# Kernel optimization log

Hardware: AMD Instinct MI355X
Metric: run time of the kernel (lower is better)

Reference implementation:

```python
import math
import jax, jax.numpy as jnp
import numpy as np

B, T, H = 4, 2048, 1024
E, K, F = 8, 2, 2048
CAP_FACTOR = 1.25


def setup_inputs() -> dict:
    key = jax.random.key(0)
    k1, k2, k3, k4 = jax.random.split(key, 4)
    x = jax.random.normal(k1, (B, T, H), dtype=jnp.float32)
    Wg = jax.random.normal(k2, (H, E), dtype=jnp.float32) * 0.02
    W_in = jax.random.normal(k3, (E, H, 2 * F), dtype=jnp.float32) * (1.0 / math.sqrt(H))
    W_out = jax.random.normal(k4, (E, F, H), dtype=jnp.float32) * (1.0 / math.sqrt(F))
    return {"x": x, "Wg": Wg, "W_in": W_in, "W_out": W_out}


def _moe_forward(x, Wg, W_in, W_out):
    b, t, h = x.shape
    xf = x.reshape(-1, h)                      # [S, H] flattened tokens
    S = xf.shape[0]
    C = int(math.ceil(K * S / E * CAP_FACTOR))  # per-expert capacity (drop_tokens=True)

    # --- gating (noiseless top-k, eval/RSample-off path) ---
    logits = xf @ Wg                           # [S, E]
    probs = jax.nn.softmax(logits, axis=-1)
    top_vals, top_idx = jax.lax.top_k(probs, K)  # [S, K]

    # --- capacity-ordered locations, slot-major priority (slot0 before slot1) ---
    flat_idx = top_idx.T.reshape(-1)           # [K*S], slot-major
    onehot = jax.nn.one_hot(flat_idx, E, dtype=jnp.int32)
    cum = jnp.cumsum(onehot, axis=0) - 1       # position within each expert
    loc = jnp.take_along_axis(cum, flat_idx[:, None], axis=1)[:, 0]
    loc = loc.reshape(K, S).T                  # [S, K]
    keep = loc < C                             # token-drop mask

    # --- gate weights normalized over kept slots (DeepSpeed top-k normalization) ---
    gates = top_vals * keep.astype(top_vals.dtype)       # [S, K]
    denom = jnp.maximum(gates.sum(-1, keepdims=True), 1e-9)
    gates = gates / denom

    # --- dispatch: scatter tokens into [E, C, H] buffers (pad slot C for drops) ---
    loc_c = jnp.where(keep, loc, C)
    e_flat = top_idx.reshape(-1)               # [S*K]
    l_flat = loc_c.reshape(-1)
    xk = jnp.broadcast_to(xf[:, None, :], (S, K, h)).reshape(-1, h)
    xk = jnp.where(keep.reshape(-1, 1), xk, 0.0)
    buf = jnp.zeros((E, C + 1, h), x.dtype).at[e_flat, l_flat].set(xk)
    inp = buf[:, :C]                           # [E, C, H]

    # --- GLU experts as grouped GEMMs ---
    hid = jnp.einsum('ech,ehf->ecf', inp, W_in)          # [E, C, 2F]
    a, g = jnp.split(hid, 2, axis=-1)
    hid = jax.nn.gelu(a, approximate=False) * g          # torch gelu = exact erf
    out_e = jnp.einsum('ecf,efh->ech', hid, W_out)       # [E, C, H]

    # --- combine: gather per-slot expert outputs, weight by gates, sum over k ---
    out_pad = jnp.concatenate([out_e, jnp.zeros((E, 1, h), out_e.dtype)], axis=1)
    gathered = out_pad[e_flat, l_flat].reshape(S, K, h)
    y = (gathered * gates[..., None]).sum(axis=1)        # [S, H]
    return y.reshape(b, t, h)


def reference(x, Wg, W_in, W_out):
    return _moe_forward(x, Wg, W_in, W_out)
```

## Files before the change

### kernel.cpp

```cpp
#include <hip/hip_runtime.h>
#include <hip/hip_bf16.h>
#include <math.h>

#define S_TOK 8192
#define HDIM  1024
#define FDIM  2048
#define CAP   2560

typedef unsigned short u16;
typedef short  s16x8 __attribute__((ext_vector_type(8)));
typedef float  f32x4 __attribute__((ext_vector_type(4)));

__device__ __forceinline__ u16 f2b(float f){
  unsigned u = __builtin_bit_cast(unsigned, f);
  u = (u + 0x7FFFu + ((u >> 16) & 1u)) >> 16;
  return (u16)u;
}
__device__ __forceinline__ float b2f(u16 h){
  unsigned u = ((unsigned)h) << 16;
  return __builtin_bit_cast(float, u);
}
__device__ __forceinline__ void gl_lds16(const u16* g, u16* l){
  auto gp = (const __attribute__((address_space(1))) unsigned int*)g;
  auto lp = (__attribute__((address_space(3))) unsigned int*)l;
  __builtin_amdgcn_global_load_lds(gp, lp, 16, 0, 0);
}

__device__ __forceinline__ int glu_reorder(int c){
  int h = (c >= 2048) ? 1 : 0;
  int cc = c - (h << 11);
  return ((cc >> 5) << 6) + (h << 5) + (cc & 31);
}

template<int REORDER>
__global__ __launch_bounds__(256) void k_transpose(const float* __restrict__ in,
                                                   u16* __restrict__ out, int R, int Cc){
  __shared__ float tile[32][33];
  int e = blockIdx.z;
  const float* ip = in + (size_t)e * R * Cc;
  u16* op = out + (size_t)e * R * Cc;
  int c0 = blockIdx.x * 32, r0 = blockIdx.y * 32;
  int tx = threadIdx.x, ty = threadIdx.y;
  #pragma unroll
  for (int j = 0; j < 32; j += 8)
    tile[ty + j][tx] = ip[(size_t)(r0 + ty + j) * Cc + c0 + tx];
  __syncthreads();
  #pragma unroll
  for (int j = 0; j < 32; j += 8){
    int c = c0 + ty + j;
    int rp = REORDER ? glu_reorder(c) : c;
    op[(size_t)rp * R + r0 + tx] = f2b(tile[tx][ty + j]);
  }
}

__global__ __launch_bounds__(256) void k_gating(const float* __restrict__ x,
                                                const float* __restrict__ Wg,
                                                int* __restrict__ eidx, float* __restrict__ vals){
  __shared__ float wgT[8][1024];
  int t = threadIdx.x;
  for (int i = t; i < 8192; i += 256) wgT[i & 7][i >> 3] = Wg[i];
  __syncthreads();
  int wid = t >> 6, l = t & 63;
  int s = blockIdx.x * 4 + wid;
  const float* xr = x + (size_t)s * HDIM;
  double acc[8] = {0,0,0,0,0,0,0,0};
  for (int j = 0; j < 16; j++){
    int h = l + 64 * j;
    float xv = xr[h];
    #pragma unroll
    for (int e = 0; e < 8; e++) acc[e] += (double)xv * (double)wgT[e][h];
  }
  #pragma unroll
  for (int off = 32; off; off >>= 1)
    #pragma unroll
    for (int e = 0; e < 8; e++) acc[e] += __shfl_down(acc[e], off);
  if (l == 0){
    double mx = acc[0];
    #pragma unroll
    for (int e = 1; e < 8; e++) mx = acc[e] > mx ? acc[e] : mx;
    double ex[8], sum = 0.0;
    #pragma unroll
    for (int e = 0; e < 8; e++){ ex[e] = exp(acc[e] - mx); sum += ex[e]; }
    double inv = 1.0 / sum;
    double p0 = -1.0; int e0 = 0;
    #pragma unroll
    for (int e = 0; e < 8; e++){ double p = ex[e] * inv; if (p > p0){ p0 = p; e0 = e; } }
    double p1 = -1.0; int e1 = 0;
    #pragma unroll
    for (int e = 0; e < 8; e++){ double p = ex[e] * inv; if (e != e0 && p > p1){ p1 = p; e1 = e; } }
    eidx[s] = e0;          vals[s] = (float)p0;
    eidx[S_TOK + s] = e1;  vals[S_TOK + s] = (float)p1;
  }
}

__global__ __launch_bounds__(1024) void k_scan(const int* __restrict__ eidx,
                                               const float* __restrict__ vals,
                                               int* __restrict__ slot, float* __restrict__ gates,
                                               int* __restrict__ cnt){
  __shared__ int sc[1024][8];
  __shared__ unsigned char keepb[2 * S_TOK];
  int t = threadIdx.x;
  int le[16];
  int c[8] = {0,0,0,0,0,0,0,0};
  #pragma unroll
  for (int j = 0; j < 16; j++){ int e = eidx[t * 16 + j]; le[j] = e; c[e]++; }
  #pragma unroll
  for (int e = 0; e < 8; e++) sc[t][e] = c[e];
  __syncthreads();
  for (int st = 1; st < 1024; st <<= 1){
    int tmp[8] = {0,0,0,0,0,0,0,0};
    bool act = (t >= st);
    if (act){
      #pragma unroll
      for (int e = 0; e < 8; e++) tmp[e] = sc[t - st][e];
    }
    __syncthreads();
    if (act){
      #pragma unroll
      for (int e = 0; e < 8; e++) sc[t][e] += tmp[e];
    }
    __syncthreads();
  }
  int run[8];
  #pragma unroll
  for (int e = 0; e < 8; e++) run[e] = t ? sc[t - 1][e] : 0;
  #pragma unroll
  for (int j = 0; j < 16; j++){
    int i = t * 16 + j; int e = le[j]; int loc = run[e]++;
    int kp = (loc < CAP);
    keepb[i] = (unsigned char)kp;
    slot[i] = kp ? (e * CAP + loc) : -1;
  }
  if (t < 8) cnt[t] = min(sc[1023][t], CAP);
  __syncthreads();
  #pragma unroll
  for (int r = 0; r < 8; r++){
    int s = t + 1024 * r;
    float g0 = keepb[s]         ? vals[s]         : 0.f;
    float g1 = keepb[S_TOK + s] ? vals[S_TOK + s] : 0.f;
    float inv = 1.f / fmaxf(g0 + g1, 1e-9f);
    gates[s] = g0 * inv;
    gates[S_TOK + s] = g1 * inv;
  }
}

__global__ __launch_bounds__(256) void k_scatter(const float* __restrict__ x,
                                                 const int* __restrict__ slot,
                                                 u16* __restrict__ A){
  int i = blockIdx.x;
  int sl = slot[i];
  if (sl < 0) return;
  int s = i & (S_TOK - 1);
  int t = threadIdx.x;
  float4 v = ((const float4*)(x + (size_t)s * HDIM))[t];
  ushort4 o; o.x = f2b(v.x); o.y = f2b(v.y); o.z = f2b(v.z); o.w = f2b(v.w);
  ((ushort4*)(A + (size_t)sl * HDIM))[t] = o;
}


#define STAGE_A(h, tt, par) { \
    const u16* gp_ = Ap + (size_t)((h)*128 + c0*8) * LDK + (size_t)(tt) * 64 + srow_off; \
    u16* lp_ = lds + (par)*16384 + (h)*8192 + c0*512; \
    gl_lds16(gp_, lp_); gl_lds16(gp_ + (size_t)8*LDK, lp_ + 512); }

#define STAGE_B(h, tt, par) { \
    const u16* gp_ = Bp + (size_t)((h)*128 + c0*8) * LDK + (size_t)(tt) * 64 + srow_off; \
    u16* lp_ = lds + 32768 + (par)*16384 + (h)*8192 + c0*512; \
    gl_lds16(gp_, lp_); gl_lds16(gp_ + (size_t)8*LDK, lp_ + 512); }

#define PH(P, KSW, NH, STAGE_CODE, POST_CODE) { \
    __builtin_amdgcn_sched_barrier(0); \
    if ((NH) == 0) { \
      _Pragma("unroll") \
      for (int m_ = 0; m_ < 8; ++m_) \
        af[m_] = *(const s16x8*)&lds[(P)*16384 + aoff + m_*1024 + (KSW)]; \
    } \
    bf[0] = *(const s16x8*)&lds[32768 + (P)*16384 + boff + (2*(NH))*1024 + (KSW)]; \
    bf[1] = *(const s16x8*)&lds[32768 + (P)*16384 + boff + (2*(NH)+1)*1024 + (KSW)]; \
    STAGE_CODE \
    __builtin_amdgcn_sched_barrier(0); __builtin_amdgcn_s_barrier(); \
    asm volatile("s_waitcnt lgkmcnt(0)" ::: "memory"); \
    __builtin_amdgcn_sched_barrier(0); \
    __builtin_amdgcn_s_setprio(1); \
    _Pragma("unroll") \
    for (int m_ = 0; m_ < 8; ++m_){ \
      acc[m_][2*(NH)]   = __builtin_amdgcn_mfma_f32_16x16x32_bf16(af[m_], bf[0], acc[m_][2*(NH)],   0, 0, 0); \
      acc[m_][2*(NH)+1] = __builtin_amdgcn_mfma_f32_16x16x32_bf16(af[m_], bf[1], acc[m_][2*(NH)+1], 0, 0, 0); \
    } \
    __builtin_amdgcn_s_setprio(0); \
    POST_CODE \
    __builtin_amdgcn_sched_barrier(0); __builtin_amdgcn_s_barrier(); }

template<int NK, int LDK, int NB, int IS_GLU>
__global__ __launch_bounds__(512, 2) void k_gemm8(const u16* __restrict__ Aall,
                                                  const u16* __restrict__ Ball,
                                                  u16* __restrict__ Out,
                                                  const int* __restrict__ cnt){
  int e = blockIdx.z, mt = blockIdx.x, nt = blockIdx.y;
  if (mt * 256 >= cnt[e]) return;
  __shared__ __align__(1024) u16 lds[65536];
  const u16* Ap = Aall + (size_t)e * CAP * LDK + (size_t)mt * 256 * LDK;
  const u16* Bp = Ball + (size_t)e * NB * LDK + (size_t)nt * 256 * LDK;

  const int t = threadIdx.x, wid = t >> 6, l = t & 63;
  const int wm = wid >> 2, wn = wid & 3;
  const int lrow = l & 15, lkhi = l >> 4;
  const int c0 = wid * 2;
  const size_t srow_off = (size_t)(l >> 3) * LDK + (size_t)(((l & 7) * 8) ^ ((l >> 3) * 8));
  const int aoff = wm * 8192 + lrow * 64;
  const int boff = (wn >> 1) * 8192 + ((wn & 1) * 64 + lrow) * 64;
  const int sx   = (l & 7) * 8;
  const int ksw0 = (lkhi * 8) ^ sx;
  const int ksw1 = (32 + lkhi * 8) ^ sx;

  f32x4 acc[8][4] = {};
  s16x8 af[8], bf[2];

  STAGE_A(0, 0, 0) STAGE_A(1, 0, 0) STAGE_B(0, 0, 0) STAGE_B(1, 0, 0)
  STAGE_A(0, 1, 1) STAGE_A(1, 1, 1)
  asm volatile("s_waitcnt vmcnt(4)" ::: "memory");
  __builtin_amdgcn_sched_barrier(0); __builtin_amdgcn_s_barrier();

  #pragma unroll 1
  for (int t2 = 0; t2 < NK / 2; ++t2){
    const int te = 2 * t2;
    const bool nl = (t2 < NK / 2 - 1);
    PH(0, ksw0, 0, { STAGE_B(0, te + 1, 1) }, {})
    PH(0, ksw0, 1, { STAGE_B(1, te + 1, 1) }, {})
    PH(0, ksw1, 0, {}, {})
    PH(0, ksw1, 1,
       { if (nl){ STAGE_A(0, te + 2, 0) STAGE_A(1, te + 2, 0) } },
       { if (nl){ asm volatile("s_waitcnt vmcnt(4)" ::: "memory"); }
         else   { asm volatile("s_waitcnt vmcnt(0)" ::: "memory"); } })
    PH(1, ksw0, 0, { if (nl){ STAGE_B(0, te + 2, 0) } }, {})
    PH(1, ksw0, 1, { if (nl){ STAGE_B(1, te + 2, 0) } }, {})
    PH(1, ksw1, 0, {}, {})
    PH(1, ksw1, 1,
       { if (nl){ STAGE_A(0, te + 3, 1) STAGE_A(1, te + 3, 1) } },
       { if (nl){ asm volatile("s_waitcnt vmcnt(4)" ::: "memory"); } })
  }

  const int rowb = mt * 256 + wm * 128 + lkhi * 4;
  if (IS_GLU){
    u16* hp = Out + (size_t)e * CAP * FDIM;
    const int colb = (nt * 4 + wn) * 32 + lrow;
    #pragma unroll
    for (int m = 0; m < 8; ++m)
      #pragma unroll
      for (int np = 0; np < 2; ++np)
        #pragma unroll
        for (int r = 0; r < 4; ++r){
          size_t row = (size_t)(rowb + m * 16 + r);
          float a = acc[m][np][r], g = acc[m][np + 2][r];
          float h = 0.5f * a * (1.f + erff(a * 0.70710678118f)) * g;
          hp[row * FDIM + colb + np * 16] = f2b(h);
        }
  } else {
    u16* op = Out + (size_t)e * CAP * HDIM;
    const int colb = nt * 256 + wn * 64 + lrow;
    #pragma unroll
    for (int m = 0; m < 8; ++m)
      #pragma unroll
      for (int n = 0; n < 4; ++n)
        #pragma unroll
        for (int r = 0; r < 4; ++r){
          size_t row = (size_t)(rowb + m * 16 + r);
          op[row * HDIM + colb + n * 16] = f2b(acc[m][n][r]);
        }
  }
}

__global__ __launch_bounds__(256) void k_gather(const u16* __restrict__ oute,
                                                const int* __restrict__ slot,
                                                const float* __restrict__ gates,
                                                float* __restrict__ y){
  int s = blockIdx.x, t = threadIdx.x;
  int s0 = slot[s], s1 = slot[S_TOK + s];
  float g0 = gates[s], g1 = gates[S_TOK + s];
  float4 r; r.x = r.y = r.z = r.w = 0.f;
  if (s0 >= 0){
    ushort4 v = ((const ushort4*)(oute + (size_t)s0 * HDIM))[t];
    r.x += g0 * b2f(v.x); r.y += g0 * b2f(v.y); r.z += g0 * b2f(v.z); r.w += g0 * b2f(v.w);
  }
  if (s1 >= 0){
    ushort4 v = ((const ushort4*)(oute + (size_t)s1 * HDIM))[t];
    r.x += g1 * b2f(v.x); r.y += g1 * b2f(v.y); r.z += g1 * b2f(v.z); r.w += g1 * b2f(v.w);
  }
  ((float4*)(y + (size_t)s * HDIM))[t] = r;
}

extern "C" void kernel_launch(void* const* d_in, const int* in_sizes, int n_in,
                              void* d_out, int out_size, void* d_ws, size_t ws_size,
                              hipStream_t stream){
  (void)in_sizes; (void)n_in; (void)out_size; (void)ws_size;
  const float* x     = (const float*)d_in[0];
  const float* Wg    = (const float*)d_in[1];
  const float* W_in  = (const float*)d_in[2];
  const float* W_out = (const float*)d_in[3];
  float* y = (float*)d_out;

  char* ws = (char*)d_ws;
  u16* WiT   = (u16*)(ws);
  u16* WoT   = (u16*)(ws + 67108864);
  u16* Ainp  = (u16*)(ws + 100663296);
  u16* hid   = (u16*)(ws + 142606336);
  int*   eidx  = (int*)  (ws + 226492416);
  float* vals  = (float*)(ws + 226492416 + 65536);
  int*   slot  = (int*)  (ws + 226492416 + 131072);
  float* gates = (float*)(ws + 226492416 + 196608);
  int*   cnt   = (int*)  (ws + 226492416 + 262144);

  k_transpose<1><<<dim3(128, 32, 8), dim3(32, 8), 0, stream>>>(W_in,  WiT, 1024, 4096);
  k_transpose<0><<<dim3(32, 64, 8),  dim3(32, 8), 0, stream>>>(W_out, WoT, 2048, 1024);
  k_gating   <<<dim3(2048), dim3(256),  0, stream>>>(x, Wg, eidx, vals);
  k_scan     <<<dim3(1),    dim3(1024), 0, stream>>>(eidx, vals, slot, gates, cnt);
  k_scatter  <<<dim3(2 * S_TOK), dim3(256), 0, stream>>>(x, slot, Ainp);
  k_gemm8<16, 1024, 4096, 1><<<dim3(10, 16, 8), dim3(512), 0, stream>>>(Ainp, WiT, hid, cnt);
  k_gemm8<32, 2048, 1024, 0><<<dim3(10, 4, 8),  dim3(512), 0, stream>>>(hid, WoT, Ainp, cnt);
  k_gather   <<<dim3(S_TOK), dim3(256), 0, stream>>>(Ainp, slot, gates, y);
}
```

Measured before the change: 644.4 us.

## Fuse combine into down-proj GEMM with atomics, tanh GELU, XCD-aware block remap

Removes the separate gather kernel by having the second GEMM scatter gate-weighted results into y with float atomicAdd, using a reverse slot-to-token map built in the scan kernel and a memset of y. Replaces the exact erf GELU with a tanh approximation. Remaps workgroup IDs so that consecutive tiles are spread across the 8 XCDs for better L2 locality. The atomics add contention and make the result order nondeterministic, and the tanh GELU changes numerics relative to the exact-erf reference.

```diff
diff --git a/kernel.cpp b/kernel.cpp
--- a/kernel.cpp
+++ b/kernel.cpp
@@ -24,6 +24,13 @@
   auto gp = (const __attribute__((address_space(1))) unsigned int*)g;
   auto lp = (__attribute__((address_space(3))) unsigned int*)l;
   __builtin_amdgcn_global_load_lds(gp, lp, 16, 0, 0);
+}
+__device__ __forceinline__ float gelu_t(float a){
+  float z = 0.7978845608f * a * (1.f + 0.044715f * a * a);
+  float e = __expf(-2.f * fabsf(z));
+  float th = (1.f - e) / (1.f + e);
+  th = (z < 0.f) ? -th : th;
+  return 0.5f * a * (1.f + th);
 }
 
 __device__ __forceinline__ int glu_reorder(int c){
@@ -96,7 +103,7 @@
 __global__ __launch_bounds__(1024) void k_scan(const int* __restrict__ eidx,
                                                const float* __restrict__ vals,
                                                int* __restrict__ slot, float* __restrict__ gates,
-                                               int* __restrict__ cnt){
+                                               int* __restrict__ cnt, int* __restrict__ rev){
   __shared__ int sc[1024][8];
   __shared__ unsigned char keepb[2 * S_TOK];
   int t = threadIdx.x;
@@ -129,7 +136,9 @@
     int i = t * 16 + j; int e = le[j]; int loc = run[e]++;
     int kp = (loc < CAP);
     keepb[i] = (unsigned char)kp;
-    slot[i] = kp ? (e * CAP + loc) : -1;
+    int sl = kp ? (e * CAP + loc) : -1;
+    slot[i] = sl;
+    if (kp) rev[sl] = i;
   }
   if (t < 8) cnt[t] = min(sc[1023][t], CAP);
   __syncthreads();
@@ -191,12 +200,23 @@
     POST_CODE \
     __builtin_amdgcn_sched_barrier(0); __builtin_amdgcn_s_barrier(); }
 
-template<int NK, int LDK, int NB, int IS_GLU>
+template<int NK, int LDK, int NB, int IS_GLU, int FUSE>
 __global__ __launch_bounds__(512, 2) void k_gemm8(const u16* __restrict__ Aall,
                                                   const u16* __restrict__ Ball,
                                                   u16* __restrict__ Out,
-                                                  const int* __restrict__ cnt){
-  int e = blockIdx.z, mt = blockIdx.x, nt = blockIdx.y;
+                                                  float* __restrict__ yout,
+                                                  const int* __restrict__ cnt,
+                                                  const int* __restrict__ rev,
+                                                  const float* __restrict__ gates){
+  const int gx = gridDim.x, gy = gridDim.y;
+  const int o = blockIdx.x + gx * (blockIdx.y + gy * blockIdx.z);
+  const int nwg = gx * gy * (int)gridDim.z;
+  const int q = nwg >> 3;
+  const int w = (o & 7) * q + (o >> 3);
+  const int mt = w % gx;
+  const int t1 = w / gx;
+  const int nt = t1 % gy;
+  const int e  = t1 / gy;
   if (mt * 256 >= cnt[e]) return;
   __shared__ __align__(1024) u16 lds[65536];
   const u16* Ap = Aall + (size_t)e * CAP * LDK + (size_t)mt * 256 * LDK;
@@ -252,9 +272,26 @@
         for (int r = 0; r < 4; ++r){
           size_t row = (size_t)(rowb + m * 16 + r);
           float a = acc[m][np][r], g = acc[m][np + 2][r];
-          float h = 0.5f * a * (1.f + erff(a * 0.70710678118f)) * g;
-          hp[row * FDIM + colb + np * 16] = f2b(h);
+          hp[row * FDIM + colb + np * 16] = f2b(gelu_t(a) * g);
         }
+  } else if (FUSE){
+    const int cE = cnt[e];
+    const int colb = nt * 256 + wn * 64 + lrow;
+    #pragma unroll
+    for (int m = 0; m < 8; ++m)
+      #pragma unroll
+      for (int r = 0; r < 4; ++r){
+        int row = rowb + m * 16 + r;
+        if (row < cE){
+          int i = rev[e * CAP + row];
+          float g = gates[i];
+          int s = i & (S_TOK - 1);
+          float* yp = yout + (size_t)s * HDIM + colb;
+          #pragma unroll
+          for (int n = 0; n < 4; ++n)
+            atomicAdd(yp + n * 16, g * acc[m][n][r]);
+        }
+      }
   } else {
     u16* op = Out + (size_t)e * CAP * HDIM;
     const int colb = nt * 256 + wn * 64 + lrow;
@@ -270,29 +307,10 @@
   }
 }
 
-__global__ __launch_bounds__(256) void k_gather(const u16* __restrict__ oute,
-                                                const int* __restrict__ slot,
-                                                const float* __restrict__ gates,
-                                                float* __restrict__ y){
-  int s = blockIdx.x, t = threadIdx.x;
-  int s0 = slot[s], s1 = slot[S_TOK + s];
-  float g0 = gates[s], g1 = gates[S_TOK + s];
-  float4 r; r.x = r.y = r.z = r.w = 0.f;
-  if (s0 >= 0){
-    ushort4 v = ((const ushort4*)(oute + (size_t)s0 * HDIM))[t];
-    r.x += g0 * b2f(v.x); r.y += g0 * b2f(v.y); r.z += g0 * b2f(v.z); r.w += g0 * b2f(v.w);
-  }
-  if (s1 >= 0){
-    ushort4 v = ((const ushort4*)(oute + (size_t)s1 * HDIM))[t];
-    r.x += g1 * b2f(v.x); r.y += g1 * b2f(v.y); r.z += g1 * b2f(v.z); r.w += g1 * b2f(v.w);
-  }
-  ((float4*)(y + (size_t)s * HDIM))[t] = r;
-}
-
 extern "C" void kernel_launch(void* const* d_in, const int* in_sizes, int n_in,
                               void* d_out, int out_size, void* d_ws, size_t ws_size,
                               hipStream_t stream){
-  (void)in_sizes; (void)n_in; (void)out_size; (void)ws_size;
+  (void)in_sizes; (void)n_in; (void)ws_size;
   const float* x     = (const float*)d_in[0];
   const float* Wg    = (const float*)d_in[1];
   const float* W_in  = (const float*)d_in[2];
@@ -309,13 +327,14 @@
   int*   slot  = (int*)  (ws + 226492416 + 131072);
   float* gates = (float*)(ws + 226492416 + 196608);
   int*   cnt   = (int*)  (ws + 226492416 + 262144);
-
+  int*   rev   = (int*)  (ws + 226492416 + 266240);
+
+  hipMemsetAsync(y, 0, (size_t)out_size * sizeof(float), stream);
   k_transpose<1><<<dim3(128, 32, 8), dim3(32, 8), 0, stream>>>(W_in,  WiT, 1024, 4096);
   k_transpose<0><<<dim3(32, 64, 8),  dim3(32, 8), 0, stream>>>(W_out, WoT, 2048, 1024);
   k_gating   <<<dim3(2048), dim3(256),  0, stream>>>(x, Wg, eidx, vals);
-  k_scan     <<<dim3(1),    dim3(1024), 0, stream>>>(eidx, vals, slot, gates, cnt);
+  k_scan     <<<dim3(1),    dim3(1024), 0, stream>>>(eidx, vals, slot, gates, cnt, rev);
   k_scatter  <<<dim3(2 * S_TOK), dim3(256), 0, stream>>>(x, slot, Ainp);
-  k_gemm8<16, 1024, 4096, 1><<<dim3(10, 16, 8), dim3(512), 0, stream>>>(Ainp, WiT, hid, cnt);
-  k_gemm8<32, 2048, 1024, 0><<<dim3(10, 4, 8),  dim3(512), 0, stream>>>(hid, WoT, Ainp, cnt);
-  k_gather   <<<dim3(S_TOK), dim3(256), 0, stream>>>(Ainp, slot, gates, y);
-}
+  k_gemm8<16, 1024, 4096, 1, 0><<<dim3(10, 16, 8), dim3(512), 0, stream>>>(Ainp, WiT, hid, y, cnt, rev, gates);
+  k_gemm8<32, 2048, 1024, 0, 1><<<dim3(10, 4, 8),  dim3(512), 0, stream>>>(hid, WoT, (u16*)nullptr, y, cnt, rev, gates);
+}
```

New measurement: 671.7 us. 4.2% more time.

## Vectorize transposes, use wave-level scan, relax GEMM barriers, swizzle workgroups, approximate GELU

Applied to the files above, without the earlier changes.

Several independent changes. The weight transpose now uses 64x64 tiles with float4 loads and ushort4 stores. Gating reads Wg directly with vector loads instead of staging it in LDS, and the single-block scan uses wave shuffles plus a small cross-wave pass in place of a 1024-step LDS Hillis-Steele scan. The GEMM drops sched_barriers and waits on lgkmcnt only on tail phases, and remaps workgroup ids across the 8 XCDs. It also replaces exact erf GELU with the tanh approximation, which differs numerically from the erf reference and may affect accuracy tolerance.

```diff
diff --git a/kernel.cpp b/kernel.cpp
--- a/kernel.cpp
+++ b/kernel.cpp
@@ -25,6 +25,13 @@
   auto lp = (__attribute__((address_space(3))) unsigned int*)l;
   __builtin_amdgcn_global_load_lds(gp, lp, 16, 0, 0);
 }
+__device__ __forceinline__ float gelu_t(float a){
+  float z = 0.7978845608f * a * (1.f + 0.044715f * a * a);
+  float e = __expf(-2.f * fabsf(z));
+  float th = (1.f - e) / (1.f + e);
+  th = (z < 0.f) ? -th : th;
+  return 0.5f * a * (1.f + th);
+}
 
 __device__ __forceinline__ int glu_reorder(int c){
   int h = (c >= 2048) ? 1 : 0;
@@ -35,40 +42,54 @@
 template<int REORDER>
 __global__ __launch_bounds__(256) void k_transpose(const float* __restrict__ in,
                                                    u16* __restrict__ out, int R, int Cc){
-  __shared__ float tile[32][33];
+  __shared__ float tl[64][65];
   int e = blockIdx.z;
   const float* ip = in + (size_t)e * R * Cc;
   u16* op = out + (size_t)e * R * Cc;
-  int c0 = blockIdx.x * 32, r0 = blockIdx.y * 32;
-  int tx = threadIdx.x, ty = threadIdx.y;
-  #pragma unroll
-  for (int j = 0; j < 32; j += 8)
-    tile[ty + j][tx] = ip[(size_t)(r0 + ty + j) * Cc + c0 + tx];
+  int c0 = blockIdx.x * 64, r0 = blockIdx.y * 64;
+  int t = threadIdx.x;
+  int tx = t & 15, ty = t >> 4;
+  #pragma unroll
+  for (int p = 0; p < 4; p++){
+    int r = ty + p * 16;
+    float4 v = *(const float4*)&ip[(size_t)(r0 + r) * Cc + c0 + tx * 4];
+    tl[r][tx * 4 + 0] = v.x; tl[r][tx * 4 + 1] = v.y;
+    tl[r][tx * 4 + 2] = v.z; tl[r][tx * 4 + 3] = v.w;
+  }
   __syncthreads();
   #pragma unroll
-  for (int j = 0; j < 32; j += 8){
-    int c = c0 + ty + j;
+  for (int p = 0; p < 4; p++){
+    int cc = ty + p * 16;
+    int c = c0 + cc;
     int rp = REORDER ? glu_reorder(c) : c;
-    op[(size_t)rp * R + r0 + tx] = f2b(tile[tx][ty + j]);
+    int rr = tx * 4;
+    ushort4 o;
+    o.x = f2b(tl[rr + 0][cc]); o.y = f2b(tl[rr + 1][cc]);
+    o.z = f2b(tl[rr + 2][cc]); o.w = f2b(tl[rr + 3][cc]);
+    *(ushort4*)&op[(size_t)rp * R + r0 + rr] = o;
   }
 }
 
 __global__ __launch_bounds__(256) void k_gating(const float* __restrict__ x,
                                                 const float* __restrict__ Wg,
                                                 int* __restrict__ eidx, float* __restrict__ vals){
-  __shared__ float wgT[8][1024];
-  int t = threadIdx.x;
-  for (int i = t; i < 8192; i += 256) wgT[i & 7][i >> 3] = Wg[i];
-  __syncthreads();
-  int wid = t >> 6, l = t & 63;
+  int t = threadIdx.x, wid = t >> 6, l = t & 63;
   int s = blockIdx.x * 4 + wid;
-  const float* xr = x + (size_t)s * HDIM;
+  const float4* xr = (const float4*)(x + (size_t)s * HDIM);
+  const float4* wg = (const float4*)Wg;
   double acc[8] = {0,0,0,0,0,0,0,0};
-  for (int j = 0; j < 16; j++){
-    int h = l + 64 * j;
-    float xv = xr[h];
-    #pragma unroll
-    for (int e = 0; e < 8; e++) acc[e] += (double)xv * (double)wgT[e][h];
+  #pragma unroll
+  for (int j4 = 0; j4 < 4; j4++){
+    float4 xv = xr[l * 4 + j4];
+    float xa[4] = {xv.x, xv.y, xv.z, xv.w};
+    #pragma unroll
+    for (int q = 0; q < 4; q++){
+      int h = l * 16 + j4 * 4 + q;
+      float4 w0 = wg[h * 2], w1 = wg[h * 2 + 1];
+      double xd = (double)xa[q];
+      acc[0] += xd * w0.x; acc[1] += xd * w0.y; acc[2] += xd * w0.z; acc[3] += xd * w0.w;
+      acc[4] += xd * w1.x; acc[5] += xd * w1.y; acc[6] += xd * w1.z; acc[7] += xd * w1.w;
+    }
   }
   #pragma unroll
   for (int off = 32; off; off >>= 1)
@@ -97,33 +118,37 @@
                                                const float* __restrict__ vals,
                                                int* __restrict__ slot, float* __restrict__ gates,
                                                int* __restrict__ cnt){
-  __shared__ int sc[1024][8];
+  __shared__ int wavetot[16][9];
+  __shared__ int waveoff[16][9];
   __shared__ unsigned char keepb[2 * S_TOK];
-  int t = threadIdx.x;
+  int t = threadIdx.x, w = t >> 6, l = t & 63;
   int le[16];
   int c[8] = {0,0,0,0,0,0,0,0};
   #pragma unroll
   for (int j = 0; j < 16; j++){ int e = eidx[t * 16 + j]; le[j] = e; c[e]++; }
-  #pragma unroll
-  for (int e = 0; e < 8; e++) sc[t][e] = c[e];
+  int inc[8];
+  #pragma unroll
+  for (int e = 0; e < 8; e++) inc[e] = c[e];
+  #pragma unroll
+  for (int off = 1; off < 64; off <<= 1)
+    #pragma unroll
+    for (int e = 0; e < 8; e++){
+      int v = __shfl_up(inc[e], off);
+      if (l >= off) inc[e] += v;
+    }
+  if (l == 63)
+    #pragma unroll
+    for (int e = 0; e < 8; e++) wavetot[w][e] = inc[e];
   __syncthreads();
-  for (int st = 1; st < 1024; st <<= 1){
-    int tmp[8] = {0,0,0,0,0,0,0,0};
-    bool act = (t >= st);
-    if (act){
-      #pragma unroll
-      for (int e = 0; e < 8; e++) tmp[e] = sc[t - st][e];
-    }
-    __syncthreads();
-    if (act){
-      #pragma unroll
-      for (int e = 0; e < 8; e++) sc[t][e] += tmp[e];
-    }
-    __syncthreads();
-  }
+  if (t < 8){
+    int run = 0;
+    for (int ww = 0; ww < 16; ww++){ waveoff[ww][t] = run; run += wavetot[ww][t]; }
+    cnt[t] = min(run, CAP);
+  }
+  __syncthreads();
   int run[8];
   #pragma unroll
-  for (int e = 0; e < 8; e++) run[e] = t ? sc[t - 1][e] : 0;
+  for (int e = 0; e < 8; e++) run[e] = waveoff[w][e] + (inc[e] - c[e]);
   #pragma unroll
   for (int j = 0; j < 16; j++){
     int i = t * 16 + j; int e = le[j]; int loc = run[e]++;
@@ -131,7 +156,6 @@
     keepb[i] = (unsigned char)kp;
     slot[i] = kp ? (e * CAP + loc) : -1;
   }
-  if (t < 8) cnt[t] = min(sc[1023][t], CAP);
   __syncthreads();
   #pragma unroll
   for (int r = 0; r < 8; r++){
@@ -168,8 +192,9 @@
     u16* lp_ = lds + 32768 + (par)*16384 + (h)*8192 + c0*512; \
     gl_lds16(gp_, lp_); gl_lds16(gp_ + (size_t)8*LDK, lp_ + 512); }
 
-#define PH(P, KSW, NH, STAGE_CODE, POST_CODE) { \
-    __builtin_amdgcn_sched_barrier(0); \
+#define CFENCE asm volatile("" ::: "memory");
+
+#define PH(P, KSW, NH, STAGE_CODE, TAILWAIT, POST_CODE) { \
     if ((NH) == 0) { \
       _Pragma("unroll") \
       for (int m_ = 0; m_ < 8; ++m_) \
@@ -178,9 +203,7 @@
     bf[0] = *(const s16x8*)&lds[32768 + (P)*16384 + boff + (2*(NH))*1024 + (KSW)]; \
     bf[1] = *(const s16x8*)&lds[32768 + (P)*16384 + boff + (2*(NH)+1)*1024 + (KSW)]; \
     STAGE_CODE \
-    __builtin_amdgcn_sched_barrier(0); __builtin_amdgcn_s_barrier(); \
-    asm volatile("s_waitcnt lgkmcnt(0)" ::: "memory"); \
-    __builtin_amdgcn_sched_barrier(0); \
+    CFENCE __builtin_amdgcn_s_barrier(); CFENCE \
     __builtin_amdgcn_s_setprio(1); \
     _Pragma("unroll") \
     for (int m_ = 0; m_ < 8; ++m_){ \
@@ -188,15 +211,24 @@
       acc[m_][2*(NH)+1] = __builtin_amdgcn_mfma_f32_16x16x32_bf16(af[m_], bf[1], acc[m_][2*(NH)+1], 0, 0, 0); \
     } \
     __builtin_amdgcn_s_setprio(0); \
+    if (TAILWAIT){ asm volatile("s_waitcnt lgkmcnt(0)" ::: "memory"); } \
     POST_CODE \
-    __builtin_amdgcn_sched_barrier(0); __builtin_amdgcn_s_barrier(); }
+    CFENCE __builtin_amdgcn_s_barrier(); CFENCE }
 
 template<int NK, int LDK, int NB, int IS_GLU>
 __global__ __launch_bounds__(512, 2) void k_gemm8(const u16* __restrict__ Aall,
                                                   const u16* __restrict__ Ball,
                                                   u16* __restrict__ Out,
                                                   const int* __restrict__ cnt){
-  int e = blockIdx.z, mt = blockIdx.x, nt = blockIdx.y;
+  const int gx = gridDim.x, gy = gridDim.y;
+  const int o = blockIdx.x + gx * (blockIdx.y + gy * blockIdx.z);
+  const int nwg = gx * gy * (int)gridDim.z;
+  const int q = nwg >> 3;
+  const int w = (o & 7) * q + (o >> 3);
+  const int mt = w % gx;
+  const int t1 = w / gx;
+  const int nt = t1 % gy;
+  const int e  = t1 / gy;
   if (mt * 256 >= cnt[e]) return;
   __shared__ __align__(1024) u16 lds[65536];
   const u16* Ap = Aall + (size_t)e * CAP * LDK + (size_t)mt * 256 * LDK;
@@ -219,24 +251,26 @@
   STAGE_A(0, 0, 0) STAGE_A(1, 0, 0) STAGE_B(0, 0, 0) STAGE_B(1, 0, 0)
   STAGE_A(0, 1, 1) STAGE_A(1, 1, 1)
   asm volatile("s_waitcnt vmcnt(4)" ::: "memory");
-  __builtin_amdgcn_sched_barrier(0); __builtin_amdgcn_s_barrier();
+  CFENCE __builtin_amdgcn_s_barrier(); CFENCE
 
   #pragma unroll 1
   for (int t2 = 0; t2 < NK / 2; ++t2){
     const int te = 2 * t2;
     const bool nl = (t2 < NK / 2 - 1);
-    PH(0, ksw0, 0, { STAGE_B(0, te + 1, 1) }, {})
-    PH(0, ksw0, 1, { STAGE_B(1, te + 1, 1) }, {})
-    PH(0, ksw1, 0, {}, {})
+    PH(0, ksw0, 0, { STAGE_B(0, te + 1, 1) }, 0, {})
+    PH(0, ksw0, 1, { STAGE_B(1, te + 1, 1) }, 0, {})
+    PH(0, ksw1, 0, {}, 1, {})
     PH(0, ksw1, 1,
        { if (nl){ STAGE_A(0, te + 2, 0) STAGE_A(1, te + 2, 0) } },
+       1,
        { if (nl){ asm volatile("s_waitcnt vmcnt(4)" ::: "memory"); }
          else   { asm volatile("s_waitcnt vmcnt(0)" ::: "memory"); } })
-    PH(1, ksw0, 0, { if (nl){ STAGE_B(0, te + 2, 0) } }, {})
-    PH(1, ksw0, 1, { if (nl){ STAGE_B(1, te + 2, 0) } }, {})
-    PH(1, ksw1, 0, {}, {})
+    PH(1, ksw0, 0, { if (nl){ STAGE_B(0, te + 2, 0) } }, 0, {})
+    PH(1, ksw0, 1, { if (nl){ STAGE_B(1, te + 2, 0) } }, 0, {})
+    PH(1, ksw1, 0, {}, 1, {})
     PH(1, ksw1, 1,
        { if (nl){ STAGE_A(0, te + 3, 1) STAGE_A(1, te + 3, 1) } },
+       1,
        { if (nl){ asm volatile("s_waitcnt vmcnt(4)" ::: "memory"); } })
   }
 
@@ -252,8 +286,7 @@
         for (int r = 0; r < 4; ++r){
           size_t row = (size_t)(rowb + m * 16 + r);
           float a = acc[m][np][r], g = acc[m][np + 2][r];
-          float h = 0.5f * a * (1.f + erff(a * 0.70710678118f)) * g;
-          hp[row * FDIM + colb + np * 16] = f2b(h);
+          hp[row * FDIM + colb + np * 16] = f2b(gelu_t(a) * g);
         }
   } else {
     u16* op = Out + (size_t)e * CAP * HDIM;
@@ -310,8 +343,8 @@
   float* gates = (float*)(ws + 226492416 + 196608);
   int*   cnt   = (int*)  (ws + 226492416 + 262144);
 
-  k_transpose<1><<<dim3(128, 32, 8), dim3(32, 8), 0, stream>>>(W_in,  WiT, 1024, 4096);
-  k_transpose<0><<<dim3(32, 64, 8),  dim3(32, 8), 0, stream>>>(W_out, WoT, 2048, 1024);
+  k_transpose<1><<<dim3(64, 16, 8), dim3(256), 0, stream>>>(W_in,  WiT, 1024, 4096);
+  k_transpose<0><<<dim3(16, 32, 8), dim3(256), 0, stream>>>(W_out, WoT, 2048, 1024);
   k_gating   <<<dim3(2048), dim3(256),  0, stream>>>(x, Wg, eidx, vals);
   k_scan     <<<dim3(1),    dim3(1024), 0, stream>>>(eidx, vals, slot, gates, cnt);
   k_scatter  <<<dim3(2 * S_TOK), dim3(256), 0, stream>>>(x, slot, Ainp);
```

Result: faster. 616.6 us (-4.3%).
